# Optimization experiments

Measured on AMD Instinct MI355X. Metric: run time of the kernel, lower is better.

Reference implementation:

```python
import jax, jax.numpy as jnp
import numpy as np

N_EMBD = 512
N_HEAD = 8
HEAD_DIM = N_EMBD // N_HEAD
MAX_REL = 5
B, T = 8, 1024  # T must be <= 2*N_EMBD due to scores[:, :, :T, :T] slice


def setup_inputs() -> dict:
    key = jax.random.key(0)
    ks = jax.random.split(key, 10)
    C, d = N_EMBD, HEAD_DIM
    s = 1.0 / np.sqrt(C)
    return {
        "x": jax.random.normal(ks[0], (B, T, C), jnp.float32),
        # nn.Linear weights are [out, in]
        "w1_w": jax.random.normal(ks[1], (C, C), jnp.float32) * s,
        "w1_b": jnp.zeros((C,), jnp.float32),
        "w2": jax.random.uniform(ks[2], (d, 2 * C), jnp.float32, -0.001, 0.001),
        "b2": jnp.zeros((2 * C,), jnp.float32),
        "v_w": jax.random.normal(ks[3], (C, C), jnp.float32) * s,
        "v_b": jnp.zeros((C,), jnp.float32),
        "proj_w": jax.random.normal(ks[4], (C, C), jnp.float32) * s,
        "proj_b": jnp.zeros((C,), jnp.float32),
        # RelativePosition embeddings table: [2*max_rel+1, head_dim]
        "rel_v_table": jax.random.normal(ks[5], (2 * MAX_REL + 1, d), jnp.float32) * s,
    }


def reference(x, w1_w, w1_b, w2, b2, v_w, v_b, proj_w, proj_b, rel_v_table):
    Bq, Tq, C = x.shape
    H, d = N_HEAD, C // N_HEAD
    # per-position MLP synthesizer scores: relu(w1(x)) [B,H,T,d] @ w2 [d,2C] + b2
    relu_out = jax.nn.relu(x @ w1_w.T + w1_b).reshape(Bq, Tq, H, d).transpose(0, 2, 1, 3)
    scores = (relu_out @ w2 + b2)[:, :, :, :Tq]  # [B,H,T,T]
    causal = jnp.tril(jnp.ones((Tq, Tq), dtype=bool))
    scores = jnp.where(causal[None, None], scores, jnp.float32(-1e10))
    prob_attn = jax.nn.softmax(scores, axis=-1)
    # standard value path
    v = (x @ v_w.T + v_b).reshape(Bq, Tq, H, d).transpose(0, 2, 1, 3)  # [B,H,T,d]
    y1 = prob_attn @ v  # [B,H,T,d]
    # relative-position value path: table lookup per (q,k) pair
    dist = jnp.arange(Tq)[None, :] - jnp.arange(Tq)[:, None]
    idx = jnp.clip(dist, -MAX_REL, 0) + MAX_REL  # [T,T] in [0, 2*MAX_REL]
    v2 = rel_v_table[idx]  # [T,T,d]
    y2 = jnp.einsum('bhqk,qkd->bhqd', prob_attn, v2)
    y = (y1 + y2).transpose(0, 2, 1, 3).reshape(Bq, Tq, C)
    return y @ proj_w.T + proj_b
```

## Files before the change

kernel.cpp:

```cpp
#include <hip/hip_runtime.h>
#include <cstdint>

#define B_ 8
#define T_ 1024
#define C_ 512
#define H_ 8

typedef __attribute__((ext_vector_type(8))) short bf16x8;
typedef __attribute__((ext_vector_type(4))) float f32x4;

__device__ __forceinline__ unsigned short f2bf(float f) {
  uint32_t u = __float_as_uint(f);
  u += 0x7FFFu + ((u >> 16) & 1u);
  return (unsigned short)(u >> 16);
}
__device__ __forceinline__ float bf2f(unsigned short h) {
  return __uint_as_float(((uint32_t)h) << 16);
}

__device__ __forceinline__ void gload16(const void* g, void* lds) {
  __builtin_amdgcn_global_load_lds(
      (const __attribute__((address_space(1))) void*)g,
      (__attribute__((address_space(3))) void*)lds, 16, 0, 0);
}

__global__ __launch_bounds__(256) void prep_all(
    const float* __restrict__ x, const float* __restrict__ w1,
    const float* __restrict__ vw, const float* __restrict__ pw,
    const float* __restrict__ w2,
    unsigned short* __restrict__ xb, unsigned short* __restrict__ w1b,
    unsigned short* __restrict__ vwb, unsigned short* __restrict__ pjb,
    unsigned short* __restrict__ w2t)
{
  __shared__ float tile[32][33];
  const int bb = blockIdx.x, t = threadIdx.x;
  if (bb < 4096) {
    int i = bb * 256 + t;
    float4 f = reinterpret_cast<const float4*>(x)[i];
    uint2 o;
    o.x = (uint32_t)f2bf(f.x) | ((uint32_t)f2bf(f.y) << 16);
    o.y = (uint32_t)f2bf(f.z) | ((uint32_t)f2bf(f.w) << 16);
    reinterpret_cast<uint2*>(xb)[i] = o;
  } else if (bb < 4864) {
    int seg = (bb - 4096) >> 8;
    int i = ((bb - 4096) & 255) * 256 + t;
    const float* in = (seg == 0) ? w1 : (seg == 1) ? vw : pw;
    unsigned short* o = (seg == 0) ? w1b : (seg == 1) ? vwb : pjb;
    float4 f = reinterpret_cast<const float4*>(in)[i];
    uint2 u;
    u.x = (uint32_t)f2bf(f.x) | ((uint32_t)f2bf(f.y) << 16);
    u.y = (uint32_t)f2bf(f.z) | ((uint32_t)f2bf(f.w) << 16);
    reinterpret_cast<uint2*>(o)[i] = u;
  } else {
    int tt = bb - 4864;
    int c0 = (tt & 31) * 32, r0 = (tt >> 5) * 32;
    int ri = t >> 3, ci = (t & 7) * 4;
    float4 f = *reinterpret_cast<const float4*>(&w2[(size_t)(r0 + ri) * 1024 + c0 + ci]);
    tile[ri][ci] = f.x; tile[ri][ci + 1] = f.y;
    tile[ri][ci + 2] = f.z; tile[ri][ci + 3] = f.w;
    __syncthreads();
    int co = t >> 3, ro = (t & 7) * 4;
    uint2 o;
    o.x = (uint32_t)f2bf(tile[ro][co])     | ((uint32_t)f2bf(tile[ro + 1][co]) << 16);
    o.y = (uint32_t)f2bf(tile[ro + 2][co]) | ((uint32_t)f2bf(tile[ro + 3][co]) << 16);
    *reinterpret_cast<uint2*>(&w2t[(size_t)(c0 + co) * 64 + r0 + ro]) = o;
  }
}

__device__ __forceinline__ void stg_w1v(
    const unsigned short* xb, const unsigned short* w1b, const unsigned short* vwb,
    char* X, char* W1, char* V, int m0, int n0, int k0, int w, int lrow, int lcol)
{
  #pragma unroll
  for (int cc = 0; cc < 10; ++cc) {
    int c = w * 10 + cc;
    if (c < 8)
      gload16(&xb[(size_t)(m0 + c * 8 + lrow) * 512 + k0 + lcol], X + c * 1024);
    else if (c < 24)
      gload16(&w1b[(size_t)(n0 + (c - 8) * 8 + lrow) * 512 + k0 + lcol], W1 + (c - 8) * 1024);
    else
      gload16(&vwb[(size_t)(n0 + (c - 24) * 8 + lrow) * 512 + k0 + lcol], V + (c - 24) * 1024);
  }
}

__global__ __launch_bounds__(256) void gemm_w1v(
    const unsigned short* __restrict__ xb,
    const unsigned short* __restrict__ w1b, const unsigned short* __restrict__ vwb,
    const float* __restrict__ w1_bias, const float* __restrict__ v_bias,
    unsigned short* __restrict__ rb, unsigned short* __restrict__ vT)
{
  __shared__ alignas(16) unsigned short Xs[2][64 * 64];
  __shared__ alignas(16) unsigned short W1s[2][128 * 64];
  __shared__ alignas(16) unsigned short Vs[2][128 * 64];

  const int tid = threadIdx.x;
  const int lane = tid & 63, w = tid >> 6;
  const int l15 = lane & 15, g4 = lane >> 4;
  const int wr = w >> 1, wc = w & 1;
  const int n0 = blockIdx.x * 128;
  const int m0 = blockIdx.y * 64;
  const int lrow = lane >> 3, lcol = (lane & 7) * 8;

  f32x4 a1[2][4] = {};
  f32x4 a2[2][4] = {};

  stg_w1v(xb, w1b, vwb, (char*)Xs[0], (char*)W1s[0], (char*)Vs[0],
          m0, n0, 0, w, lrow, lcol);

  for (int t = 0; t < 8; ++t) {
    __syncthreads();
    if (t < 7)
      stg_w1v(xb, w1b, vwb, (char*)Xs[(t + 1) & 1], (char*)W1s[(t + 1) & 1],
              (char*)Vs[(t + 1) & 1], m0, n0, (t + 1) * 64, w, lrow, lcol);
    const char* Xc  = (const char*)Xs[t & 1];
    const char* W1c = (const char*)W1s[t & 1];
    const char* Vc  = (const char*)Vs[t & 1];
    #pragma unroll
    for (int ks = 0; ks < 2; ++ks) {
      bf16x8 af[2], wf[4], vf[4];
      #pragma unroll
      for (int i = 0; i < 2; ++i)
        af[i] = *(const bf16x8*)(Xc + (wr * 32 + 16 * i + l15) * 128 + ks * 64 + g4 * 16);
      #pragma unroll
      for (int j = 0; j < 4; ++j) {
        int n = wc * 64 + 16 * j + l15;
        wf[j] = *(const bf16x8*)(W1c + n * 128 + ks * 64 + g4 * 16);
        vf[j] = *(const bf16x8*)(Vc  + n * 128 + ks * 64 + g4 * 16);
      }
      #pragma unroll
      for (int i = 0; i < 2; ++i)
        #pragma unroll
        for (int j = 0; j < 4; ++j) {
          a1[i][j] = __builtin_amdgcn_mfma_f32_16x16x32_bf16(af[i], wf[j], a1[i][j], 0, 0, 0);
          a2[i][j] = __builtin_amdgcn_mfma_f32_16x16x32_bf16(af[i], vf[j], a2[i][j], 0, 0, 0);
        }
    }
  }

  #pragma unroll
  for (int i = 0; i < 2; ++i) {
    int mb = m0 + wr * 32 + 16 * i + g4 * 4;
    #pragma unroll
    for (int j = 0; j < 4; ++j) {
      int n = n0 + wc * 64 + 16 * j + l15;
      float b1 = w1_bias[n];
      #pragma unroll
      for (int rg = 0; rg < 4; ++rg)
        rb[(size_t)(mb + rg) * 512 + n] = f2bf(fmaxf(a1[i][j][rg] + b1, 0.f));
      float bv = v_bias[n];
      unsigned short p[4];
      #pragma unroll
      for (int rg = 0; rg < 4; ++rg) p[rg] = f2bf(a2[i][j][rg] + bv);
      *reinterpret_cast<uint2*>(&vT[(size_t)n * 8192 + mb]) =
          *reinterpret_cast<const uint2*>(p);
    }
  }
}

__device__ __forceinline__ void stg_proj(
    const unsigned short* A, const unsigned short* Wb,
    char* As, char* Ws, int m0, int n0, int k0, int w, int lrow, int lcol)
{
  #pragma unroll
  for (int cc = 0; cc < 6; ++cc) {
    int c = w * 6 + cc;
    if (c < 8)
      gload16(&A[(size_t)(m0 + c * 8 + lrow) * 512 + k0 + lcol], As + c * 1024);
    else
      gload16(&Wb[(size_t)(n0 + (c - 8) * 8 + lrow) * 512 + k0 + lcol], Ws + (c - 8) * 1024);
  }
}

__global__ __launch_bounds__(256) void gemm_proj(
    const unsigned short* __restrict__ A, const unsigned short* __restrict__ Wb,
    const float* __restrict__ bias, float* __restrict__ out)
{
  __shared__ alignas(16) unsigned short As[2][64 * 64];
  __shared__ alignas(16) unsigned short Ws[2][128 * 64];

  const int tid = threadIdx.x;
  const int lane = tid & 63, w = tid >> 6;
  const int l15 = lane & 15, g4 = lane >> 4;
  const int wr = w >> 1, wc = w & 1;
  const int n0 = blockIdx.x * 128;
  const int m0 = blockIdx.y * 64;
  const int lrow = lane >> 3, lcol = (lane & 7) * 8;

  f32x4 acc[2][4] = {};

  stg_proj(A, Wb, (char*)As[0], (char*)Ws[0], m0, n0, 0, w, lrow, lcol);

  for (int t = 0; t < 8; ++t) {
    __syncthreads();
    if (t < 7)
      stg_proj(A, Wb, (char*)As[(t + 1) & 1], (char*)Ws[(t + 1) & 1],
               m0, n0, (t + 1) * 64, w, lrow, lcol);
    const char* Ac = (const char*)As[t & 1];
    const char* Wc = (const char*)Ws[t & 1];
    #pragma unroll
    for (int ks = 0; ks < 2; ++ks) {
      bf16x8 af[2], wf[4];
      #pragma unroll
      for (int i = 0; i < 2; ++i)
        af[i] = *(const bf16x8*)(Ac + (wr * 32 + 16 * i + l15) * 128 + ks * 64 + g4 * 16);
      #pragma unroll
      for (int j = 0; j < 4; ++j)
        wf[j] = *(const bf16x8*)(Wc + (wc * 64 + 16 * j + l15) * 128 + ks * 64 + g4 * 16);
      #pragma unroll
      for (int i = 0; i < 2; ++i)
        #pragma unroll
        for (int j = 0; j < 4; ++j)
          acc[i][j] = __builtin_amdgcn_mfma_f32_16x16x32_bf16(af[i], wf[j], acc[i][j], 0, 0, 0);
    }
  }

  #pragma unroll
  for (int i = 0; i < 2; ++i) {
    int mb = m0 + wr * 32 + 16 * i + g4 * 4;
    #pragma unroll
    for (int j = 0; j < 4; ++j) {
      int n = n0 + wc * 64 + 16 * j + l15;
      float bj = bias[n];
      #pragma unroll
      for (int rg = 0; rg < 4; ++rg)
        out[(size_t)(mb + rg) * 512 + n] = acc[i][j][rg] + bj;
    }
  }
}

#define SA_VLOAD(K0)                                                                  \
  do {                                                                                \
    { int c = tid;       int row = c >> 3, sl = c & 7;                                \
      w0 = *reinterpret_cast<const uint4*>(&w2t[(size_t)((K0) + row) * 64 + sl * 8]); } \
    { int c = tid + 256; int row = c >> 3, sl = c & 7;                                \
      w1 = *reinterpret_cast<const uint4*>(&w2t[(size_t)((K0) + row) * 64 + sl * 8]); } \
    { int c = tid;       int row = c >> 3, sl = c & 7;                                \
      v0 = *reinterpret_cast<const uint4*>(&vT[(size_t)(h * 64 + row) * 8192 + b * 1024 + (K0) + sl * 8]); } \
    { int c = tid + 256; int row = c >> 3, sl = c & 7;                                \
      v1 = *reinterpret_cast<const uint4*>(&vT[(size_t)(h * 64 + row) * 8192 + b * 1024 + (K0) + sl * 8]); } \
  } while (0)

#define SA_VSTORE(W2B, VTB)                                                           \
  do {                                                                                \
    { int c = tid;       int row = c >> 3, sl = c & 7;                                \
      *reinterpret_cast<uint4*>((char*)(W2B) + row * 128 + ((sl ^ (row & 7)) << 4)) = w0; } \
    { int c = tid + 256; int row = c >> 3, sl = c & 7;                                \
      *reinterpret_cast<uint4*>((char*)(W2B) + row * 128 + ((sl ^ (row & 7)) << 4)) = w1; } \
    { int c = tid;       int row = c >> 3, sl = c & 7;                                \
      *reinterpret_cast<uint4*>((char*)(VTB) + row * 128 + ((sl ^ (row & 7)) << 4)) = v0; } \
    { int c = tid + 256; int row = c >> 3, sl = c & 7;                                \
      *reinterpret_cast<uint4*>((char*)(VTB) + row * 128 + ((sl ^ (row & 7)) << 4)) = v1; } \
  } while (0)

__global__ __launch_bounds__(256) void synth_attn_mfma(
    const unsigned short* __restrict__ rb, const unsigned short* __restrict__ vT,
    const unsigned short* __restrict__ w2t, const float* __restrict__ b2,
    const float* __restrict__ table, unsigned short* __restrict__ ya)
{
  __shared__ alignas(16) unsigned short RtS[64 * 64];
  __shared__ alignas(16) unsigned short ElS[64 * 64];
  __shared__ alignas(16) unsigned short W2S[2][64 * 64];
  __shared__ alignas(16) unsigned short VtS[2][80 * 64];
  __shared__ float tap[64][5];
  __shared__ float tabs[6][64];

  char* Rt = (char*)RtS;
  char* El = (char*)ElS;

  const int tid = threadIdx.x;
  const int lane = tid & 63, w = tid >> 6;
  const int l15 = lane & 15, g = lane >> 4;
  const int bid = blockIdx.x;
  const int pp = bid & 7;
  const int bh = bid >> 3;
  const int b = bh >> 3, h = bh & 7;
  const int qrl = 16 * w + l15;
  const int sx = l15 & 7;

  #pragma unroll
  for (int t2 = 0; t2 < 2; ++t2) {
    int idx = tid + t2 * 256;
    if (idx < 384) ((float*)tabs)[idx] = table[idx];
  }
  {
    int row = 64 + (tid >> 4), ch = tid & 15;
    uint2 val;
    val.x = (row == 64) ? 0x3F803F80u : 0u;
    val.y = val.x;
    *reinterpret_cast<uint2*>((char*)VtS[0] + row * 128 + ch * 8) = val;
    *reinterpret_cast<uint2*>((char*)VtS[1] + row * 128 + ch * 8) = val;
  }

  uint4 w0, w1, v0, v1;

  for (int half = 0; half < 2; ++half) {
    const int qt = half ? (15 - pp) : pp;
    const int q0 = qt * 64;

    __syncthreads();
    #pragma unroll
    for (int t2 = 0; t2 < 2; ++t2) {
      int c = tid + t2 * 256; int row = c >> 3, sl = c & 7;
      uint4 d = *reinterpret_cast<const uint4*>(
          &rb[(size_t)(b * 1024 + q0 + row) * 512 + h * 64 + sl * 8]);
      *reinterpret_cast<uint4*>(Rt + row * 128 + ((sl ^ (row & 7)) << 4)) = d;
    }
    if (lane < 16) {
      int qr = w * 16 + lane;
      #pragma unroll
      for (int jj = 0; jj < 5; ++jj) tap[qr][jj] = 0.f;
    }

    f32x4 acc[4] = {};
    f32x4 accS = {};

    SA_VLOAD(0);
    SA_VSTORE(W2S[0], VtS[0]);

    for (int kt = 0; kt <= qt; ++kt) {
      const int k0 = kt * 64;
      const int cur = kt & 1;
      __syncthreads();

      float4 bq0 = *reinterpret_cast<const float4*>(&b2[k0 +  0 + 4 * g]);
      float4 bq1 = *reinterpret_cast<const float4*>(&b2[k0 + 16 + 4 * g]);
      float4 bq2 = *reinterpret_cast<const float4*>(&b2[k0 + 32 + 4 * g]);
      float4 bq3 = *reinterpret_cast<const float4*>(&b2[k0 + 48 + 4 * g]);
      if (kt < qt) SA_VLOAD(k0 + 64);

      const char* W2c = (const char*)W2S[cur];
      const char* Vtc = (const char*)VtS[cur];

      bf16x8 rb0 = *(const bf16x8*)(Rt + qrl * 128 + ((g ^ sx) << 4));
      bf16x8 rb1 = *(const bf16x8*)(Rt + qrl * 128 + (((4 + g) ^ sx) << 4));
      f32x4 sf[4] = {};
      #pragma unroll
      for (int j = 0; j < 4; ++j) {
        int ar = 16 * j + l15;
        bf16x8 wa0 = *(const bf16x8*)(W2c + ar * 128 + ((g ^ sx) << 4));
        bf16x8 wa1 = *(const bf16x8*)(W2c + ar * 128 + (((4 + g) ^ sx) << 4));
        sf[j] = __builtin_amdgcn_mfma_f32_16x16x32_bf16(wa0, rb0, sf[j], 0, 0, 0);
        sf[j] = __builtin_amdgcn_mfma_f32_16x16x32_bf16(wa1, rb1, sf[j], 0, 0, 0);
      }

      const bool diag = (kt == qt);
      #pragma unroll
      for (int j = 0; j < 4; ++j) {
        const float4 bq = (j == 0) ? bq0 : (j == 1) ? bq1 : (j == 2) ? bq2 : bq3;
        const int kb = 16 * j + 4 * g;
        float e0 = __expf(sf[j][0] + bq.x);
        float e1 = __expf(sf[j][1] + bq.y);
        float e2 = __expf(sf[j][2] + bq.z);
        float e3 = __expf(sf[j][3] + bq.w);
        if (diag) {
          e0 = (kb + 0 <= qrl) ? e0 : 0.f;
          e1 = (kb + 1 <= qrl) ? e1 : 0.f;
          e2 = (kb + 2 <= qrl) ? e2 : 0.f;
          e3 = (kb + 3 <= qrl) ? e3 : 0.f;
        }
        uint2 pk;
        pk.x = (uint32_t)f2bf(e0) | ((uint32_t)f2bf(e1) << 16);
        pk.y = (uint32_t)f2bf(e2) | ((uint32_t)f2bf(e3) << 16);
        int slot = (2 * j + (g >> 1)) ^ sx;
        *reinterpret_cast<uint2*>(El + qrl * 128 + slot * 16 + (g & 1) * 8) = pk;
      }

      bf16x8 ae0 = *(const bf16x8*)(El + qrl * 128 + ((g ^ sx) << 4));
      bf16x8 ae1 = *(const bf16x8*)(El + qrl * 128 + (((4 + g) ^ sx) << 4));
      #pragma unroll
      for (int j = 0; j < 4; ++j) {
        int vr = 16 * j + l15;
        bf16x8 vb0 = *(const bf16x8*)(Vtc + vr * 128 + ((g ^ sx) << 4));
        bf16x8 vb1 = *(const bf16x8*)(Vtc + vr * 128 + (((4 + g) ^ sx) << 4));
        acc[j] = __builtin_amdgcn_mfma_f32_16x16x32_bf16(ae0, vb0, acc[j], 0, 0, 0);
        acc[j] = __builtin_amdgcn_mfma_f32_16x16x32_bf16(ae1, vb1, acc[j], 0, 0, 0);
      }
      {
        int orow = 64 + l15;
        bf16x8 o0 = *(const bf16x8*)(Vtc + orow * 128 + ((g ^ sx) << 4));
        bf16x8 o1 = *(const bf16x8*)(Vtc + orow * 128 + (((4 + g) ^ sx) << 4));
        accS = __builtin_amdgcn_mfma_f32_16x16x32_bf16(ae0, o0, accS, 0, 0, 0);
        accS = __builtin_amdgcn_mfma_f32_16x16x32_bf16(ae1, o1, accS, 0, 0, 0);
      }

      if (lane < 16) {
        int qr = w * 16 + lane;
        int off = q0 + qr - 4 - k0;
        #pragma unroll
        for (int jj = 0; jj < 5; ++jj) {
          int kk = off + jj;
          if ((unsigned)kk < 64u) {
            int byte = qr * 128 + ((((kk >> 3) ^ (qr & 7)) << 4) | ((kk & 7) << 1));
            tap[qr][jj] += bf2f(*reinterpret_cast<unsigned short*>(El + byte));
          }
        }
      }

      if (kt < qt) SA_VSTORE(W2S[(kt + 1) & 1], VtS[(kt + 1) & 1]);
    }

    float inv[4], tp[4][5];
    #pragma unroll
    for (int rr = 0; rr < 4; ++rr) {
      float ls = __shfl(accS[rr], lane & 48, 64);
      inv[rr] = 1.f / ls;
      int qr = w * 16 + g * 4 + rr;
      #pragma unroll
      for (int jj = 0; jj < 5; ++jj) tp[rr][jj] = tap[qr][jj] * inv[rr];
    }
    #pragma unroll
    for (int j = 0; j < 4; ++j) {
      int dd = 16 * j + l15;
      float t0 = tabs[0][dd];
      float dt[5];
      #pragma unroll
      for (int jj = 0; jj < 5; ++jj) dt[jj] = tabs[jj + 1][dd] - t0;
      #pragma unroll
      for (int rr = 0; rr < 4; ++rr) {
        int qr = w * 16 + g * 4 + rr;
        float y = acc[j][rr] * inv[rr] + t0;
        #pragma unroll
        for (int jj = 0; jj < 5; ++jj) y = fmaf(tp[rr][jj], dt[jj], y);
        ya[(size_t)(b * 1024 + q0 + qr) * 512 + h * 64 + dd] = f2bf(y);
      }
    }
  }
}

extern "C" void kernel_launch(void* const* d_in, const int* in_sizes, int n_in,
                              void* d_out, int out_size, void* d_ws, size_t ws_size,
                              hipStream_t stream) {
  const float* x      = (const float*)d_in[0];
  const float* w1_w   = (const float*)d_in[1];
  const float* w1_b   = (const float*)d_in[2];
  const float* w2     = (const float*)d_in[3];
  const float* b2     = (const float*)d_in[4];
  const float* v_w    = (const float*)d_in[5];
  const float* v_b    = (const float*)d_in[6];
  const float* proj_w = (const float*)d_in[7];
  const float* proj_b = (const float*)d_in[8];
  const float* relv   = (const float*)d_in[9];
  float* out = (float*)d_out;

  const size_t buf = (size_t)B_ * T_ * C_;
  const size_t wsz = (size_t)C_ * C_;
  unsigned short* rb    = (unsigned short*)d_ws;
  unsigned short* vT    = rb + buf;
  unsigned short* xb    = vT + buf;
  unsigned short* yab   = xb + buf;
  unsigned short* w1b   = yab + buf;
  unsigned short* vwb   = w1b + wsz;
  unsigned short* projb = vwb + wsz;
  unsigned short* w2t   = projb + wsz;

  prep_all<<<4928, 256, 0, stream>>>(x, w1_w, v_w, proj_w, w2,
                                     xb, w1b, vwb, projb, w2t);

  gemm_w1v<<<dim3(4, 128), 256, 0, stream>>>(xb, w1b, vwb, w1_b, v_b, rb, vT);

  synth_attn_mfma<<<512, 256, 0, stream>>>(rb, vT, w2t, b2, relv, yab);

  gemm_proj<<<dim3(4, 128), 256, 0, stream>>>(yab, projb, proj_b, out);
}
```

Before: 142.5 us.

## Drop double buffering, shrink GEMM tiles, and split attention into one block per query tile

Removes LDS double buffering from the two projection GEMMs and the synthesizer attention kernel, replacing it with simple load-sync-compute loops. GEMM N-tiles shrink from 128 to 64, which doubles the grid. The attention kernel now launches one block per query tile, ordered longest-first, instead of pairing short and long tiles in a single block. This raises parallelism and lowers LDS use, but exposes global-load latency and gives unequal per-block work in attention.

```diff
diff --git a/kernel.cpp b/kernel.cpp
--- a/kernel.cpp
+++ b/kernel.cpp
@@ -67,70 +67,61 @@
   }
 }
 
-__device__ __forceinline__ void stg_w1v(
-    const unsigned short* xb, const unsigned short* w1b, const unsigned short* vwb,
-    char* X, char* W1, char* V, int m0, int n0, int k0, int w, int lrow, int lcol)
-{
-  #pragma unroll
-  for (int cc = 0; cc < 10; ++cc) {
-    int c = w * 10 + cc;
-    if (c < 8)
-      gload16(&xb[(size_t)(m0 + c * 8 + lrow) * 512 + k0 + lcol], X + c * 1024);
-    else if (c < 24)
-      gload16(&w1b[(size_t)(n0 + (c - 8) * 8 + lrow) * 512 + k0 + lcol], W1 + (c - 8) * 1024);
-    else
-      gload16(&vwb[(size_t)(n0 + (c - 24) * 8 + lrow) * 512 + k0 + lcol], V + (c - 24) * 1024);
-  }
-}
-
 __global__ __launch_bounds__(256) void gemm_w1v(
     const unsigned short* __restrict__ xb,
     const unsigned short* __restrict__ w1b, const unsigned short* __restrict__ vwb,
     const float* __restrict__ w1_bias, const float* __restrict__ v_bias,
     unsigned short* __restrict__ rb, unsigned short* __restrict__ vT)
 {
-  __shared__ alignas(16) unsigned short Xs[2][64 * 64];
-  __shared__ alignas(16) unsigned short W1s[2][128 * 64];
-  __shared__ alignas(16) unsigned short Vs[2][128 * 64];
+  __shared__ alignas(16) unsigned short Xs[64 * 64];
+  __shared__ alignas(16) unsigned short W1s[64 * 64];
+  __shared__ alignas(16) unsigned short Vs[64 * 64];
 
   const int tid = threadIdx.x;
   const int lane = tid & 63, w = tid >> 6;
   const int l15 = lane & 15, g4 = lane >> 4;
   const int wr = w >> 1, wc = w & 1;
-  const int n0 = blockIdx.x * 128;
+  const int n0 = blockIdx.x * 64;
   const int m0 = blockIdx.y * 64;
   const int lrow = lane >> 3, lcol = (lane & 7) * 8;
 
-  f32x4 a1[2][4] = {};
-  f32x4 a2[2][4] = {};
-
-  stg_w1v(xb, w1b, vwb, (char*)Xs[0], (char*)W1s[0], (char*)Vs[0],
-          m0, n0, 0, w, lrow, lcol);
+  f32x4 a1[2][2] = {};
+  f32x4 a2[2][2] = {};
 
   for (int t = 0; t < 8; ++t) {
-    __syncthreads();
-    if (t < 7)
-      stg_w1v(xb, w1b, vwb, (char*)Xs[(t + 1) & 1], (char*)W1s[(t + 1) & 1],
-              (char*)Vs[(t + 1) & 1], m0, n0, (t + 1) * 64, w, lrow, lcol);
-    const char* Xc  = (const char*)Xs[t & 1];
-    const char* W1c = (const char*)W1s[t & 1];
-    const char* Vc  = (const char*)Vs[t & 1];
+    const int k0 = t * 64;
+    __syncthreads();
+    #pragma unroll
+    for (int cc = 0; cc < 6; ++cc) {
+      int c = w * 6 + cc;
+      if (c < 8)
+        gload16(&xb[(size_t)(m0 + c * 8 + lrow) * 512 + k0 + lcol], (char*)Xs + c * 1024);
+      else if (c < 16)
+        gload16(&w1b[(size_t)(n0 + (c - 8) * 8 + lrow) * 512 + k0 + lcol],
+                (char*)W1s + (c - 8) * 1024);
+      else
+        gload16(&vwb[(size_t)(n0 + (c - 16) * 8 + lrow) * 512 + k0 + lcol],
+                (char*)Vs + (c - 16) * 1024);
+    }
+    __syncthreads();
+
     #pragma unroll
     for (int ks = 0; ks < 2; ++ks) {
-      bf16x8 af[2], wf[4], vf[4];
+      bf16x8 af[2], wf[2], vf[2];
       #pragma unroll
       for (int i = 0; i < 2; ++i)
-        af[i] = *(const bf16x8*)(Xc + (wr * 32 + 16 * i + l15) * 128 + ks * 64 + g4 * 16);
-      #pragma unroll
-      for (int j = 0; j < 4; ++j) {
-        int n = wc * 64 + 16 * j + l15;
-        wf[j] = *(const bf16x8*)(W1c + n * 128 + ks * 64 + g4 * 16);
-        vf[j] = *(const bf16x8*)(Vc  + n * 128 + ks * 64 + g4 * 16);
+        af[i] = *(const bf16x8*)((const char*)Xs +
+                 (wr * 32 + 16 * i + l15) * 128 + ks * 64 + g4 * 16);
+      #pragma unroll
+      for (int j = 0; j < 2; ++j) {
+        int n = wc * 32 + 16 * j + l15;
+        wf[j] = *(const bf16x8*)((const char*)W1s + n * 128 + ks * 64 + g4 * 16);
+        vf[j] = *(const bf16x8*)((const char*)Vs  + n * 128 + ks * 64 + g4 * 16);
       }
       #pragma unroll
       for (int i = 0; i < 2; ++i)
         #pragma unroll
-        for (int j = 0; j < 4; ++j) {
+        for (int j = 0; j < 2; ++j) {
           a1[i][j] = __builtin_amdgcn_mfma_f32_16x16x32_bf16(af[i], wf[j], a1[i][j], 0, 0, 0);
           a2[i][j] = __builtin_amdgcn_mfma_f32_16x16x32_bf16(af[i], vf[j], a2[i][j], 0, 0, 0);
         }
@@ -141,8 +132,8 @@
   for (int i = 0; i < 2; ++i) {
     int mb = m0 + wr * 32 + 16 * i + g4 * 4;
     #pragma unroll
-    for (int j = 0; j < 4; ++j) {
-      int n = n0 + wc * 64 + 16 * j + l15;
+    for (int j = 0; j < 2; ++j) {
+      int n = n0 + wc * 32 + 16 * j + l15;
       float b1 = w1_bias[n];
       #pragma unroll
       for (int rg = 0; rg < 4; ++rg)
@@ -157,59 +148,52 @@
   }
 }
 
-__device__ __forceinline__ void stg_proj(
-    const unsigned short* A, const unsigned short* Wb,
-    char* As, char* Ws, int m0, int n0, int k0, int w, int lrow, int lcol)
-{
-  #pragma unroll
-  for (int cc = 0; cc < 6; ++cc) {
-    int c = w * 6 + cc;
-    if (c < 8)
-      gload16(&A[(size_t)(m0 + c * 8 + lrow) * 512 + k0 + lcol], As + c * 1024);
-    else
-      gload16(&Wb[(size_t)(n0 + (c - 8) * 8 + lrow) * 512 + k0 + lcol], Ws + (c - 8) * 1024);
-  }
-}
-
 __global__ __launch_bounds__(256) void gemm_proj(
     const unsigned short* __restrict__ A, const unsigned short* __restrict__ Wb,
     const float* __restrict__ bias, float* __restrict__ out)
 {
-  __shared__ alignas(16) unsigned short As[2][64 * 64];
-  __shared__ alignas(16) unsigned short Ws[2][128 * 64];
+  __shared__ alignas(16) unsigned short As[64 * 64];
+  __shared__ alignas(16) unsigned short Ws[64 * 64];
 
   const int tid = threadIdx.x;
   const int lane = tid & 63, w = tid >> 6;
   const int l15 = lane & 15, g4 = lane >> 4;
   const int wr = w >> 1, wc = w & 1;
-  const int n0 = blockIdx.x * 128;
+  const int n0 = blockIdx.x * 64;
   const int m0 = blockIdx.y * 64;
   const int lrow = lane >> 3, lcol = (lane & 7) * 8;
 
-  f32x4 acc[2][4] = {};
-
-  stg_proj(A, Wb, (char*)As[0], (char*)Ws[0], m0, n0, 0, w, lrow, lcol);
+  f32x4 acc[2][2] = {};
 
   for (int t = 0; t < 8; ++t) {
-    __syncthreads();
-    if (t < 7)
-      stg_proj(A, Wb, (char*)As[(t + 1) & 1], (char*)Ws[(t + 1) & 1],
-               m0, n0, (t + 1) * 64, w, lrow, lcol);
-    const char* Ac = (const char*)As[t & 1];
-    const char* Wc = (const char*)Ws[t & 1];
+    const int k0 = t * 64;
+    __syncthreads();
+    #pragma unroll
+    for (int cc = 0; cc < 4; ++cc) {
+      int c = w * 4 + cc;
+      if (c < 8)
+        gload16(&A[(size_t)(m0 + c * 8 + lrow) * 512 + k0 + lcol], (char*)As + c * 1024);
+      else
+        gload16(&Wb[(size_t)(n0 + (c - 8) * 8 + lrow) * 512 + k0 + lcol],
+                (char*)Ws + (c - 8) * 1024);
+    }
+    __syncthreads();
+
     #pragma unroll
     for (int ks = 0; ks < 2; ++ks) {
-      bf16x8 af[2], wf[4];
+      bf16x8 af[2], wf[2];
       #pragma unroll
       for (int i = 0; i < 2; ++i)
-        af[i] = *(const bf16x8*)(Ac + (wr * 32 + 16 * i + l15) * 128 + ks * 64 + g4 * 16);
-      #pragma unroll
-      for (int j = 0; j < 4; ++j)
-        wf[j] = *(const bf16x8*)(Wc + (wc * 64 + 16 * j + l15) * 128 + ks * 64 + g4 * 16);
+        af[i] = *(const bf16x8*)((const char*)As +
+                 (wr * 32 + 16 * i + l15) * 128 + ks * 64 + g4 * 16);
+      #pragma unroll
+      for (int j = 0; j < 2; ++j)
+        wf[j] = *(const bf16x8*)((const char*)Ws +
+                 (wc * 32 + 16 * j + l15) * 128 + ks * 64 + g4 * 16);
       #pragma unroll
       for (int i = 0; i < 2; ++i)
         #pragma unroll
-        for (int j = 0; j < 4; ++j)
+        for (int j = 0; j < 2; ++j)
           acc[i][j] = __builtin_amdgcn_mfma_f32_16x16x32_bf16(af[i], wf[j], acc[i][j], 0, 0, 0);
     }
   }
@@ -218,8 +202,8 @@
   for (int i = 0; i < 2; ++i) {
     int mb = m0 + wr * 32 + 16 * i + g4 * 4;
     #pragma unroll
-    for (int j = 0; j < 4; ++j) {
-      int n = n0 + wc * 64 + 16 * j + l15;
+    for (int j = 0; j < 2; ++j) {
+      int n = n0 + wc * 32 + 16 * j + l15;
       float bj = bias[n];
       #pragma unroll
       for (int rg = 0; rg < 4; ++rg)
@@ -240,16 +224,16 @@
       v1 = *reinterpret_cast<const uint4*>(&vT[(size_t)(h * 64 + row) * 8192 + b * 1024 + (K0) + sl * 8]); } \
   } while (0)
 
-#define SA_VSTORE(W2B, VTB)                                                           \
+#define SA_VSTORE()                                                                   \
   do {                                                                                \
     { int c = tid;       int row = c >> 3, sl = c & 7;                                \
-      *reinterpret_cast<uint4*>((char*)(W2B) + row * 128 + ((sl ^ (row & 7)) << 4)) = w0; } \
+      *reinterpret_cast<uint4*>(W2 + row * 128 + ((sl ^ (row & 7)) << 4)) = w0; }     \
     { int c = tid + 256; int row = c >> 3, sl = c & 7;                                \
-      *reinterpret_cast<uint4*>((char*)(W2B) + row * 128 + ((sl ^ (row & 7)) << 4)) = w1; } \
+      *reinterpret_cast<uint4*>(W2 + row * 128 + ((sl ^ (row & 7)) << 4)) = w1; }     \
     { int c = tid;       int row = c >> 3, sl = c & 7;                                \
-      *reinterpret_cast<uint4*>((char*)(VTB) + row * 128 + ((sl ^ (row & 7)) << 4)) = v0; } \
+      *reinterpret_cast<uint4*>(Vt + row * 128 + ((sl ^ (row & 7)) << 4)) = v0; }     \
     { int c = tid + 256; int row = c >> 3, sl = c & 7;                                \
-      *reinterpret_cast<uint4*>((char*)(VTB) + row * 128 + ((sl ^ (row & 7)) << 4)) = v1; } \
+      *reinterpret_cast<uint4*>(Vt + row * 128 + ((sl ^ (row & 7)) << 4)) = v1; }     \
   } while (0)
 
 __global__ __launch_bounds__(256) void synth_attn_mfma(
@@ -259,21 +243,24 @@
 {
   __shared__ alignas(16) unsigned short RtS[64 * 64];
   __shared__ alignas(16) unsigned short ElS[64 * 64];
-  __shared__ alignas(16) unsigned short W2S[2][64 * 64];
-  __shared__ alignas(16) unsigned short VtS[2][80 * 64];
+  __shared__ alignas(16) unsigned short W2S[64 * 64];
+  __shared__ alignas(16) unsigned short VtS[80 * 64];
   __shared__ float tap[64][5];
   __shared__ float tabs[6][64];
 
   char* Rt = (char*)RtS;
   char* El = (char*)ElS;
+  char* W2 = (char*)W2S;
+  char* Vt = (char*)VtS;
 
   const int tid = threadIdx.x;
   const int lane = tid & 63, w = tid >> 6;
   const int l15 = lane & 15, g = lane >> 4;
   const int bid = blockIdx.x;
-  const int pp = bid & 7;
-  const int bh = bid >> 3;
+  const int qt = 15 - (bid >> 6);
+  const int bh = bid & 63;
   const int b = bh >> 3, h = bh & 7;
+  const int q0 = qt * 64;
   const int qrl = 16 * w + l15;
   const int sx = l15 & 7;
 
@@ -287,142 +274,127 @@
     uint2 val;
     val.x = (row == 64) ? 0x3F803F80u : 0u;
     val.y = val.x;
-    *reinterpret_cast<uint2*>((char*)VtS[0] + row * 128 + ch * 8) = val;
-    *reinterpret_cast<uint2*>((char*)VtS[1] + row * 128 + ch * 8) = val;
-  }
+    *reinterpret_cast<uint2*>(Vt + row * 128 + ch * 8) = val;
+  }
+  #pragma unroll
+  for (int t2 = 0; t2 < 2; ++t2) {
+    int c = tid + t2 * 256; int row = c >> 3, sl = c & 7;
+    uint4 d = *reinterpret_cast<const uint4*>(
+        &rb[(size_t)(b * 1024 + q0 + row) * 512 + h * 64 + sl * 8]);
+    *reinterpret_cast<uint4*>(Rt + row * 128 + ((sl ^ (row & 7)) << 4)) = d;
+  }
+  if (lane < 16) {
+    int qr = w * 16 + lane;
+    #pragma unroll
+    for (int jj = 0; jj < 5; ++jj) tap[qr][jj] = 0.f;
+  }
+
+  f32x4 acc[4] = {};
+  f32x4 accS = {};
 
   uint4 w0, w1, v0, v1;
-
-  for (int half = 0; half < 2; ++half) {
-    const int qt = half ? (15 - pp) : pp;
-    const int q0 = qt * 64;
-
-    __syncthreads();
-    #pragma unroll
-    for (int t2 = 0; t2 < 2; ++t2) {
-      int c = tid + t2 * 256; int row = c >> 3, sl = c & 7;
-      uint4 d = *reinterpret_cast<const uint4*>(
-          &rb[(size_t)(b * 1024 + q0 + row) * 512 + h * 64 + sl * 8]);
-      *reinterpret_cast<uint4*>(Rt + row * 128 + ((sl ^ (row & 7)) << 4)) = d;
-    }
+  SA_VLOAD(0);
+
+  for (int kt = 0; kt <= qt; ++kt) {
+    const int k0 = kt * 64;
+    __syncthreads();
+    SA_VSTORE();
+    if (kt < qt) SA_VLOAD(k0 + 64);
+    float4 bq0 = *reinterpret_cast<const float4*>(&b2[k0 +  0 + 4 * g]);
+    float4 bq1 = *reinterpret_cast<const float4*>(&b2[k0 + 16 + 4 * g]);
+    float4 bq2 = *reinterpret_cast<const float4*>(&b2[k0 + 32 + 4 * g]);
+    float4 bq3 = *reinterpret_cast<const float4*>(&b2[k0 + 48 + 4 * g]);
+    __syncthreads();
+
+    bf16x8 rb0 = *(const bf16x8*)(Rt + qrl * 128 + ((g ^ sx) << 4));
+    bf16x8 rb1 = *(const bf16x8*)(Rt + qrl * 128 + (((4 + g) ^ sx) << 4));
+    f32x4 sf[4] = {};
+    #pragma unroll
+    for (int j = 0; j < 4; ++j) {
+      int ar = 16 * j + l15;
+      bf16x8 wa0 = *(const bf16x8*)(W2 + ar * 128 + ((g ^ sx) << 4));
+      bf16x8 wa1 = *(const bf16x8*)(W2 + ar * 128 + (((4 + g) ^ sx) << 4));
+      sf[j] = __builtin_amdgcn_mfma_f32_16x16x32_bf16(wa0, rb0, sf[j], 0, 0, 0);
+      sf[j] = __builtin_amdgcn_mfma_f32_16x16x32_bf16(wa1, rb1, sf[j], 0, 0, 0);
+    }
+
+    const bool diag = (kt == qt);
+    #pragma unroll
+    for (int j = 0; j < 4; ++j) {
+      const float4 bq = (j == 0) ? bq0 : (j == 1) ? bq1 : (j == 2) ? bq2 : bq3;
+      const int kb = 16 * j + 4 * g;
+      float e0 = __expf(sf[j][0] + bq.x);
+      float e1 = __expf(sf[j][1] + bq.y);
+      float e2 = __expf(sf[j][2] + bq.z);
+      float e3 = __expf(sf[j][3] + bq.w);
+      if (diag) {
+        e0 = (kb + 0 <= qrl) ? e0 : 0.f;
+        e1 = (kb + 1 <= qrl) ? e1 : 0.f;
+        e2 = (kb + 2 <= qrl) ? e2 : 0.f;
+        e3 = (kb + 3 <= qrl) ? e3 : 0.f;
+      }
+      uint2 pk;
+      pk.x = (uint32_t)f2bf(e0) | ((uint32_t)f2bf(e1) << 16);
+      pk.y = (uint32_t)f2bf(e2) | ((uint32_t)f2bf(e3) << 16);
+      int slot = (2 * j + (g >> 1)) ^ sx;
+      *reinterpret_cast<uint2*>(El + qrl * 128 + slot * 16 + (g & 1) * 8) = pk;
+    }
+
+    bf16x8 ae0 = *(const bf16x8*)(El + qrl * 128 + ((g ^ sx) << 4));
+    bf16x8 ae1 = *(const bf16x8*)(El + qrl * 128 + (((4 + g) ^ sx) << 4));
+    #pragma unroll
+    for (int j = 0; j < 4; ++j) {
+      int vr = 16 * j + l15;
+      bf16x8 vb0 = *(const bf16x8*)(Vt + vr * 128 + ((g ^ sx) << 4));
+      bf16x8 vb1 = *(const bf16x8*)(Vt + vr * 128 + (((4 + g) ^ sx) << 4));
+      acc[j] = __builtin_amdgcn_mfma_f32_16x16x32_bf16(ae0, vb0, acc[j], 0, 0, 0);
+      acc[j] = __builtin_amdgcn_mfma_f32_16x16x32_bf16(ae1, vb1, acc[j], 0, 0, 0);
+    }
+    {
+      int orow = 64 + l15;
+      bf16x8 o0 = *(const bf16x8*)(Vt + orow * 128 + ((g ^ sx) << 4));
+      bf16x8 o1 = *(const bf16x8*)(Vt + orow * 128 + (((4 + g) ^ sx) << 4));
+      accS = __builtin_amdgcn_mfma_f32_16x16x32_bf16(ae0, o0, accS, 0, 0, 0);
+      accS = __builtin_amdgcn_mfma_f32_16x16x32_bf16(ae1, o1, accS, 0, 0, 0);
+    }
+
     if (lane < 16) {
       int qr = w * 16 + lane;
-      #pragma unroll
-      for (int jj = 0; jj < 5; ++jj) tap[qr][jj] = 0.f;
-    }
-
-    f32x4 acc[4] = {};
-    f32x4 accS = {};
-
-    SA_VLOAD(0);
-    SA_VSTORE(W2S[0], VtS[0]);
-
-    for (int kt = 0; kt <= qt; ++kt) {
-      const int k0 = kt * 64;
-      const int cur = kt & 1;
-      __syncthreads();
-
-      float4 bq0 = *reinterpret_cast<const float4*>(&b2[k0 +  0 + 4 * g]);
-      float4 bq1 = *reinterpret_cast<const float4*>(&b2[k0 + 16 + 4 * g]);
-      float4 bq2 = *reinterpret_cast<const float4*>(&b2[k0 + 32 + 4 * g]);
-      float4 bq3 = *reinterpret_cast<const float4*>(&b2[k0 + 48 + 4 * g]);
-      if (kt < qt) SA_VLOAD(k0 + 64);
-
-      const char* W2c = (const char*)W2S[cur];
-      const char* Vtc = (const char*)VtS[cur];
-
-      bf16x8 rb0 = *(const bf16x8*)(Rt + qrl * 128 + ((g ^ sx) << 4));
-      bf16x8 rb1 = *(const bf16x8*)(Rt + qrl * 128 + (((4 + g) ^ sx) << 4));
-      f32x4 sf[4] = {};
-      #pragma unroll
-      for (int j = 0; j < 4; ++j) {
-        int ar = 16 * j + l15;
-        bf16x8 wa0 = *(const bf16x8*)(W2c + ar * 128 + ((g ^ sx) << 4));
-        bf16x8 wa1 = *(const bf16x8*)(W2c + ar * 128 + (((4 + g) ^ sx) << 4));
-        sf[j] = __builtin_amdgcn_mfma_f32_16x16x32_bf16(wa0, rb0, sf[j], 0, 0, 0);
-        sf[j] = __builtin_amdgcn_mfma_f32_16x16x32_bf16(wa1, rb1, sf[j], 0, 0, 0);
-      }
-
-      const bool diag = (kt == qt);
-      #pragma unroll
-      for (int j = 0; j < 4; ++j) {
-        const float4 bq = (j == 0) ? bq0 : (j == 1) ? bq1 : (j == 2) ? bq2 : bq3;
-        const int kb = 16 * j + 4 * g;
-        float e0 = __expf(sf[j][0] + bq.x);
-        float e1 = __expf(sf[j][1] + bq.y);
-        float e2 = __expf(sf[j][2] + bq.z);
-        float e3 = __expf(sf[j][3] + bq.w);
-        if (diag) {
-          e0 = (kb + 0 <= qrl) ? e0 : 0.f;
-          e1 = (kb + 1 <= qrl) ? e1 : 0.f;
-          e2 = (kb + 2 <= qrl) ? e2 : 0.f;
-          e3 = (kb + 3 <= qrl) ? e3 : 0.f;
-        }
-        uint2 pk;
-        pk.x = (uint32_t)f2bf(e0) | ((uint32_t)f2bf(e1) << 16);
-        pk.y = (uint32_t)f2bf(e2) | ((uint32_t)f2bf(e3) << 16);
-        int slot = (2 * j + (g >> 1)) ^ sx;
-        *reinterpret_cast<uint2*>(El + qrl * 128 + slot * 16 + (g & 1) * 8) = pk;
-      }
-
-      bf16x8 ae0 = *(const bf16x8*)(El + qrl * 128 + ((g ^ sx) << 4));
-      bf16x8 ae1 = *(const bf16x8*)(El + qrl * 128 + (((4 + g) ^ sx) << 4));
-      #pragma unroll
-      for (int j = 0; j < 4; ++j) {
-        int vr = 16 * j + l15;
-        bf16x8 vb0 = *(const bf16x8*)(Vtc + vr * 128 + ((g ^ sx) << 4));
-        bf16x8 vb1 = *(const bf16x8*)(Vtc + vr * 128 + (((4 + g) ^ sx) << 4));
-        acc[j] = __builtin_amdgcn_mfma_f32_16x16x32_bf16(ae0, vb0, acc[j], 0, 0, 0);
-        acc[j] = __builtin_amdgcn_mfma_f32_16x16x32_bf16(ae1, vb1, acc[j], 0, 0, 0);
-      }
-      {
-        int orow = 64 + l15;
-        bf16x8 o0 = *(const bf16x8*)(Vtc + orow * 128 + ((g ^ sx) << 4));
-        bf16x8 o1 = *(const bf16x8*)(Vtc + orow * 128 + (((4 + g) ^ sx) << 4));
-        accS = __builtin_amdgcn_mfma_f32_16x16x32_bf16(ae0, o0, accS, 0, 0, 0);
-        accS = __builtin_amdgcn_mfma_f32_16x16x32_bf16(ae1, o1, accS, 0, 0, 0);
-      }
-
-      if (lane < 16) {
-        int qr = w * 16 + lane;
-        int off = q0 + qr - 4 - k0;
-        #pragma unroll
-        for (int jj = 0; jj < 5; ++jj) {
-          int kk = off + jj;
-          if ((unsigned)kk < 64u) {
-            int byte = qr * 128 + ((((kk >> 3) ^ (qr & 7)) << 4) | ((kk & 7) << 1));
-            tap[qr][jj] += bf2f(*reinterpret_cast<unsigned short*>(El + byte));
-          }
+      int off = q0 + qr - 4 - k0;
+      #pragma unroll
+      for (int jj = 0; jj < 5; ++jj) {
+        int kk = off + jj;
+        if ((unsigned)kk < 64u) {
+          int byte = qr * 128 + ((((kk >> 3) ^ (qr & 7)) << 4) | ((kk & 7) << 1));
+          tap[qr][jj] += bf2f(*reinterpret_cast<unsigned short*>(El + byte));
         }
       }
-
-      if (kt < qt) SA_VSTORE(W2S[(kt + 1) & 1], VtS[(kt + 1) & 1]);
-    }
-
-    float inv[4], tp[4][5];
+    }
+  }
+
+  float inv[4], tp[4][5];
+  #pragma unroll
+  for (int rr = 0; rr < 4; ++rr) {
+    float ls = __shfl(accS[rr], lane & 48, 64);
+    inv[rr] = 1.f / ls;
+    int qr = w * 16 + g * 4 + rr;
+    #pragma unroll
+    for (int jj = 0; jj < 5; ++jj) tp[rr][jj] = tap[qr][jj] * inv[rr];
+  }
+  #pragma unroll
+  for (int j = 0; j < 4; ++j) {
+    int dd = 16 * j + l15;
+    float t0 = tabs[0][dd];
+    float dt[5];
+    #pragma unroll
+    for (int jj = 0; jj < 5; ++jj) dt[jj] = tabs[jj + 1][dd] - t0;
     #pragma unroll
     for (int rr = 0; rr < 4; ++rr) {
-      float ls = __shfl(accS[rr], lane & 48, 64);
-      inv[rr] = 1.f / ls;
       int qr = w * 16 + g * 4 + rr;
-      #pragma unroll
-      for (int jj = 0; jj < 5; ++jj) tp[rr][jj] = tap[qr][jj] * inv[rr];
-    }
-    #pragma unroll
-    for (int j = 0; j < 4; ++j) {
-      int dd = 16 * j + l15;
-      float t0 = tabs[0][dd];
-      float dt[5];
-      #pragma unroll
-      for (int jj = 0; jj < 5; ++jj) dt[jj] = tabs[jj + 1][dd] - t0;
-      #pragma unroll
-      for (int rr = 0; rr < 4; ++rr) {
-        int qr = w * 16 + g * 4 + rr;
-        float y = acc[j][rr] * inv[rr] + t0;
-        #pragma unroll
-        for (int jj = 0; jj < 5; ++jj) y = fmaf(tp[rr][jj], dt[jj], y);
-        ya[(size_t)(b * 1024 + q0 + qr) * 512 + h * 64 + dd] = f2bf(y);
-      }
+      float y = acc[j][rr] * inv[rr] + t0;
+      #pragma unroll
+      for (int jj = 0; jj < 5; ++jj) y = fmaf(tp[rr][jj], dt[jj], y);
+      ya[(size_t)(b * 1024 + q0 + qr) * 512 + h * 64 + dd] = f2bf(y);
     }
   }
 }
@@ -456,9 +428,9 @@
   prep_all<<<4928, 256, 0, stream>>>(x, w1_w, v_w, proj_w, w2,
                                      xb, w1b, vwb, projb, w2t);
 
-  gemm_w1v<<<dim3(4, 128), 256, 0, stream>>>(xb, w1b, vwb, w1_b, v_b, rb, vT);
-
-  synth_attn_mfma<<<512, 256, 0, stream>>>(rb, vT, w2t, b2, relv, yab);
-
-  gemm_proj<<<dim3(4, 128), 256, 0, stream>>>(yab, projb, proj_b, out);
-}
+  gemm_w1v<<<dim3(8, 128), 256, 0, stream>>>(xb, w1b, vwb, w1_b, v_b, rb, vT);
+
+  synth_attn_mfma<<<1024, 256, 0, stream>>>(rb, vT, w2t, b2, relv, yab);
+
+  gemm_proj<<<dim3(8, 128), 256, 0, stream>>>(yab, projb, proj_b, out);
+}
```

Result: no change. 144.5 us (+1.4%).
